# Kernel tuning notes

Measured on AMD Instinct MI355X. Metric: run time of the kernel, lower is better.

## Reference

```python
import jax, jax.numpy as jnp
import numpy as np

N_NODES = 50000
N_EDGES = 1600000
D = 64
F = 8
K = 16384


def setup_inputs() -> dict:
    key = jax.random.key(0)
    k1, k2, k3, k4, k5 = jax.random.split(key, 5)
    raw_data = jax.random.randint(k1, (N_NODES,), 0, F, dtype=jnp.int64) if jax.config.jax_enable_x64 else jax.random.randint(k1, (N_NODES,), 0, F, dtype=jnp.int32)
    edge_src = jax.random.randint(k2, (N_EDGES,), 0, N_NODES, dtype=jnp.int32)
    edge_dst = jax.random.randint(k3, (N_EDGES,), 0, N_NODES, dtype=jnp.int32)
    edge_vals = jax.random.normal(k4, (N_EDGES, D), dtype=jnp.float32)
    core_idxs = jax.random.randint(k5, (K,), 0, N_NODES, dtype=jnp.int32)
    return {
        "raw_data": raw_data,
        "edge_src": edge_src,
        "edge_dst": edge_dst,
        "edge_vals": edge_vals,
        "core_idxs": core_idxs,
        "feature_type_count": F,
    }


def reference(raw_data, edge_src, edge_dst, edge_vals, core_idxs, feature_type_count):
    # For each feature type f and origin node i:
    #   out[i, f, :] = max over edges (i -> j) of (edge_vals * [raw_data[j] == f])
    # Origins with no edges at all are zero (torch zero-init of max_res).
    n_nodes = raw_data.shape[0]
    dst_type = raw_data[edge_dst]  # [E] feature type of each edge's neighbor
    outs = []
    for f in range(feature_type_count):  # small fixed loop over feature types
        mask = (dst_type == f).astype(edge_vals.dtype)          # [E]
        masked = edge_vals * mask[:, None]                       # [E, D]
        seg = jax.ops.segment_max(masked, edge_src, num_segments=n_nodes)  # [N, D]
        seg = jnp.where(jnp.isneginf(seg), jnp.zeros((), seg.dtype), seg)  # empty origins -> 0
        outs.append(seg[core_idxs])                              # [K, D]
    return jnp.stack(outs, axis=1)  # [K, F, D]
```

## Files before the change

kernel.cpp:

```cpp
#include <hip/hip_runtime.h>

#define NNODES 50000
#define FT 8
#define DD 64
#define KK 16384
#define CAPF 16
#define OVFCAP 32768
#define NBW 1568


__global__ void init_kernel(int* __restrict__ cnt, int* __restrict__ bits,
                            int* __restrict__ head, int* __restrict__ gtot) {
    int i = blockIdx.x * 256 + threadIdx.x;
    if (i < NNODES * FT) cnt[i] = 0;
    if (i < NBW) bits[i] = 0;
    if (i < NNODES) head[i] = -1;
    if (i < 4) gtot[i] = 0;
}

__global__ void mark_kernel(const int* __restrict__ core, int* __restrict__ bits,
                            int* __restrict__ head, int* __restrict__ nxt,
                            int* __restrict__ slot_node, int* __restrict__ gtot) {
    int k = blockIdx.x * 256 + threadIdx.x;
    if (k >= KK) return;
    int node = core[k];
    nxt[k] = atomicExch(&head[node], k);
    unsigned bit = 1u << (node & 31);
    unsigned old = atomicOr((unsigned*)&bits[node >> 5], bit);
    if (!(old & bit)) {
        int s = atomicAdd(&gtot[1], 1);
        slot_node[s] = node;
    }
}

__global__ void scatter_kernel(const int4* __restrict__ esrc4, const int4* __restrict__ edst4,
                               const int* __restrict__ rawd, const int* __restrict__ bits,
                               int* __restrict__ cnt, int* __restrict__ sorted,
                               int* __restrict__ gtot, int* __restrict__ ovf_key,
                               int* __restrict__ ovf_e, int nE) {
    int t = blockIdx.x * 256 + threadIdx.x;
    int e = t * 4;
    if (e >= nE) return;
    if (e + 3 < nE) {
        int4 s = esrc4[t];
        int4 d = edst4[t];
        int sv[4] = {s.x, s.y, s.z, s.w};
        int dv[4] = {d.x, d.y, d.z, d.w};
#pragma unroll
        for (int j = 0; j < 4; ++j) {
            int sn = sv[j];
            if (!((((unsigned)bits[sn >> 5]) >> (sn & 31)) & 1u)) continue;
            int cell = sn * FT + rawd[dv[j]];
            int p = atomicAdd(&cnt[cell], 1);
            if (p < CAPF) {
                sorted[(size_t)cell * CAPF + p] = e + j;
            } else {
                int q = atomicAdd(&gtot[0], 1);
                if (q < OVFCAP) { ovf_key[q] = cell; ovf_e[q] = e + j; }
            }
        }
    } else {
        const int* esrc = (const int*)esrc4;
        const int* edst = (const int*)edst4;
        for (; e < nE; ++e) {
            int sn = esrc[e];
            if (!((((unsigned)bits[sn >> 5]) >> (sn & 31)) & 1u)) continue;
            int cell = sn * FT + rawd[edst[e]];
            int p = atomicAdd(&cnt[cell], 1);
            if (p < CAPF) {
                sorted[(size_t)cell * CAPF + p] = e;
            } else {
                int q = atomicAdd(&gtot[0], 1);
                if (q < OVFCAP) { ovf_key[q] = cell; ovf_e[q] = e; }
            }
        }
    }
}

#define RL(x) __builtin_amdgcn_readfirstlane(x)

__global__ void compute_kernel(const int* __restrict__ slot_node, const int* __restrict__ cnt,
                               const int* __restrict__ sorted, const int* __restrict__ head,
                               const int* __restrict__ nxt, const float* __restrict__ evals,
                               const int* __restrict__ gtot, const int* __restrict__ ovf_key,
                               const int* __restrict__ ovf_e, float* __restrict__ out) {
    int wave = (blockIdx.x * blockDim.x + threadIdx.x) >> 6;
    int lane = threadIdx.x & 63;
    if (wave >= gtot[1]) return;
    int node = RL(slot_node[wave]);

    const int4* c4 = (const int4*)(cnt + node * FT);
    int4 cA = c4[0], cB = c4[1];
    int cf[FT] = { RL(cA.x), RL(cA.y), RL(cA.z), RL(cA.w),
                   RL(cB.x), RL(cB.y), RL(cB.z), RL(cB.w) };
    int deg = 0;
    bool anyovf = false;
#pragma unroll
    for (int f = 0; f < FT; ++f) { deg += cf[f]; anyovf |= (cf[f] > CAPF); }

    const int4* bkt4 = (const int4*)(sorted + (size_t)node * FT * CAPF);
    int4 id0[FT], id1[FT];
#pragma unroll
    for (int f = 0; f < FT; ++f) { id0[f] = bkt4[f * 4]; id1[f] = bkt4[f * 4 + 1]; }

    float rmax[FT];
#pragma unroll
    for (int f = 0; f < FT; ++f) {
        int n = cf[f] < CAPF ? cf[f] : CAPF;
        float m0 = -INFINITY, m1 = -INFINITY, m2 = -INFINITY, m3 = -INFINITY;
        if (n > 0) m0 = evals[(size_t)RL(id0[f].x) * DD + lane];
        if (n > 1) m1 = evals[(size_t)RL(id0[f].y) * DD + lane];
        if (n > 2) m2 = evals[(size_t)RL(id0[f].z) * DD + lane];
        if (n > 3) m3 = evals[(size_t)RL(id0[f].w) * DD + lane];
        if (n > 4) m0 = fmaxf(m0, evals[(size_t)RL(id1[f].x) * DD + lane]);
        if (n > 5) m1 = fmaxf(m1, evals[(size_t)RL(id1[f].y) * DD + lane]);
        if (n > 6) m2 = fmaxf(m2, evals[(size_t)RL(id1[f].z) * DD + lane]);
        if (n > 7) m3 = fmaxf(m3, evals[(size_t)RL(id1[f].w) * DD + lane]);
        if (n > 8) {
            const int* bkt = sorted + ((size_t)node * FT + f) * CAPF;
            for (int i = 8; i < n; ++i)
                m0 = fmaxf(m0, evals[(size_t)RL(bkt[i]) * DD + lane]);
        }
        rmax[f] = fmaxf(fmaxf(m0, m1), fmaxf(m2, m3));
    }

    if (anyovf) {
        int no = gtot[0]; if (no > OVFCAP) no = OVFCAP;
        for (int q = 0; q < no; ++q) {
            int key = ovf_key[q];
            if ((key >> 3) != node) continue;
            int fo = key & 7;
            float v = evals[(size_t)ovf_e[q] * DD + lane];
#pragma unroll
            for (int t = 0; t < FT; ++t)
                if (t == fo) rmax[t] = fmaxf(rmax[t], v);
        }
    }

    float res[FT];
#pragma unroll
    for (int f = 0; f < FT; ++f) {
        int matched = cf[f];
        float val;
        if (matched == 0)        val = 0.0f;
        else if (matched < deg)  val = fmaxf(rmax[f], 0.0f);
        else                     val = rmax[f];
        res[f] = val;
    }

    for (int k = head[node]; k >= 0; k = nxt[k]) {
        float* op = out + (size_t)k * (FT * DD) + lane;
#pragma unroll
        for (int f = 0; f < FT; ++f) op[f * DD] = res[f];
    }
}

extern "C" void kernel_launch(void* const* d_in, const int* in_sizes, int n_in,
                              void* d_out, int out_size, void* d_ws, size_t ws_size,
                              hipStream_t stream) {
    const int*   rawd  = (const int*)d_in[0];
    const int*   esrc  = (const int*)d_in[1];
    const int*   edst  = (const int*)d_in[2];
    const float* evals = (const float*)d_in[3];
    const int*   core  = (const int*)d_in[4];
    int nE = in_sizes[1];

    int* wsi       = (int*)d_ws;
    int* cnt       = wsi;
    int* bits      = wsi + 400000;
    int* head      = wsi + 401568;
    int* nxt       = wsi + 451568;
    int* slot_node = wsi + 467952;
    int* gtot      = wsi + 484336;
    int* ovf_key   = wsi + 484340;
    int* ovf_e     = wsi + 517108;
    int* sorted    = wsi + 549888;

    init_kernel<<<(NNODES * FT + 255) / 256, 256, 0, stream>>>(cnt, bits, head, gtot);
    mark_kernel<<<(KK + 255) / 256, 256, 0, stream>>>(core, bits, head, nxt, slot_node, gtot);

    int nE4 = (nE + 3) / 4;
    scatter_kernel<<<(nE4 + 255) / 256, 256, 0, stream>>>(
        (const int4*)esrc, (const int4*)edst, rawd, bits, cnt, sorted,
        gtot, ovf_key, ovf_e, nE);

    long long cthreads = (long long)KK * 64;
    compute_kernel<<<(int)((cthreads + 255) / 256), 256, 0, stream>>>(
        slot_node, cnt, sorted, head, nxt, evals, gtot, ovf_key, ovf_e, (float*)d_out);
}
```

Measured before the change: 71.71 us.

## Replace init kernel with memset, drop slot list, widen scatter, use nontemporal accesses

Replaces the init kernel with a single hipMemsetAsync by storing linked-list heads offset by one, so zero means empty. Drops the compacted slot_node list: the compute kernel now launches one wave per node and exits early when the node's bitmap bit is clear. The scatter kernel handles 8 edges per thread instead of 4. Gathers of edge_vals and writes to the output use nontemporal load/store builtins. Together these cut a launch and some atomics, at the cost of launching about three times as many waves for compute, most of which exit immediately, and of worse ordering of node processing.

Measured after the change: 102.6 us. 1.43x slower.

```diff
diff --git a/kernel.cpp b/kernel.cpp
--- a/kernel.cpp
+++ b/kernel.cpp
@@ -9,47 +9,32 @@
 #define NBW 1568
 
 
-__global__ void init_kernel(int* __restrict__ cnt, int* __restrict__ bits,
-                            int* __restrict__ head, int* __restrict__ gtot) {
-    int i = blockIdx.x * 256 + threadIdx.x;
-    if (i < NNODES * FT) cnt[i] = 0;
-    if (i < NBW) bits[i] = 0;
-    if (i < NNODES) head[i] = -1;
-    if (i < 4) gtot[i] = 0;
-}
-
-__global__ void mark_kernel(const int* __restrict__ core, int* __restrict__ bits,
-                            int* __restrict__ head, int* __restrict__ nxt,
-                            int* __restrict__ slot_node, int* __restrict__ gtot) {
+__global__ void mark_kernel(const int* __restrict__ core, unsigned* __restrict__ bits,
+                            int* __restrict__ headp, int* __restrict__ nxtp) {
     int k = blockIdx.x * 256 + threadIdx.x;
     if (k >= KK) return;
     int node = core[k];
-    nxt[k] = atomicExch(&head[node], k);
-    unsigned bit = 1u << (node & 31);
-    unsigned old = atomicOr((unsigned*)&bits[node >> 5], bit);
-    if (!(old & bit)) {
-        int s = atomicAdd(&gtot[1], 1);
-        slot_node[s] = node;
-    }
+    nxtp[k] = atomicExch(&headp[node], k + 1);
+    atomicOr(&bits[node >> 5], 1u << (node & 31));
 }
 
 __global__ void scatter_kernel(const int4* __restrict__ esrc4, const int4* __restrict__ edst4,
-                               const int* __restrict__ rawd, const int* __restrict__ bits,
+                               const int* __restrict__ rawd, const unsigned* __restrict__ bits,
                                int* __restrict__ cnt, int* __restrict__ sorted,
                                int* __restrict__ gtot, int* __restrict__ ovf_key,
                                int* __restrict__ ovf_e, int nE) {
     int t = blockIdx.x * 256 + threadIdx.x;
-    int e = t * 4;
+    int e = t * 8;
     if (e >= nE) return;
-    if (e + 3 < nE) {
-        int4 s = esrc4[t];
-        int4 d = edst4[t];
-        int sv[4] = {s.x, s.y, s.z, s.w};
-        int dv[4] = {d.x, d.y, d.z, d.w};
+    if (e + 7 < nE) {
+        int4 sA = esrc4[t * 2], sB = esrc4[t * 2 + 1];
+        int4 dA = edst4[t * 2], dB = edst4[t * 2 + 1];
+        int sv[8] = {sA.x, sA.y, sA.z, sA.w, sB.x, sB.y, sB.z, sB.w};
+        int dv[8] = {dA.x, dA.y, dA.z, dA.w, dB.x, dB.y, dB.z, dB.w};
 #pragma unroll
-        for (int j = 0; j < 4; ++j) {
+        for (int j = 0; j < 8; ++j) {
             int sn = sv[j];
-            if (!((((unsigned)bits[sn >> 5]) >> (sn & 31)) & 1u)) continue;
+            if (!((bits[sn >> 5] >> (sn & 31)) & 1u)) continue;
             int cell = sn * FT + rawd[dv[j]];
             int p = atomicAdd(&cnt[cell], 1);
             if (p < CAPF) {
@@ -64,7 +49,7 @@
         const int* edst = (const int*)edst4;
         for (; e < nE; ++e) {
             int sn = esrc[e];
-            if (!((((unsigned)bits[sn >> 5]) >> (sn & 31)) & 1u)) continue;
+            if (!((bits[sn >> 5] >> (sn & 31)) & 1u)) continue;
             int cell = sn * FT + rawd[edst[e]];
             int p = atomicAdd(&cnt[cell], 1);
             if (p < CAPF) {
@@ -79,15 +64,15 @@
 
 #define RL(x) __builtin_amdgcn_readfirstlane(x)
 
-__global__ void compute_kernel(const int* __restrict__ slot_node, const int* __restrict__ cnt,
-                               const int* __restrict__ sorted, const int* __restrict__ head,
-                               const int* __restrict__ nxt, const float* __restrict__ evals,
+__global__ void compute_kernel(const unsigned* __restrict__ bits, const int* __restrict__ cnt,
+                               const int* __restrict__ sorted, const int* __restrict__ headp,
+                               const int* __restrict__ nxtp, const float* __restrict__ evals,
                                const int* __restrict__ gtot, const int* __restrict__ ovf_key,
                                const int* __restrict__ ovf_e, float* __restrict__ out) {
-    int wave = (blockIdx.x * blockDim.x + threadIdx.x) >> 6;
+    int node = (blockIdx.x * blockDim.x + threadIdx.x) >> 6;
     int lane = threadIdx.x & 63;
-    if (wave >= gtot[1]) return;
-    int node = RL(slot_node[wave]);
+    if (node >= NNODES) return;
+    if (!((bits[node >> 5] >> (node & 31)) & 1u)) return;
 
     const int4* c4 = (const int4*)(cnt + node * FT);
     int4 cA = c4[0], cB = c4[1];
@@ -108,18 +93,18 @@
     for (int f = 0; f < FT; ++f) {
         int n = cf[f] < CAPF ? cf[f] : CAPF;
         float m0 = -INFINITY, m1 = -INFINITY, m2 = -INFINITY, m3 = -INFINITY;
-        if (n > 0) m0 = evals[(size_t)RL(id0[f].x) * DD + lane];
-        if (n > 1) m1 = evals[(size_t)RL(id0[f].y) * DD + lane];
-        if (n > 2) m2 = evals[(size_t)RL(id0[f].z) * DD + lane];
-        if (n > 3) m3 = evals[(size_t)RL(id0[f].w) * DD + lane];
-        if (n > 4) m0 = fmaxf(m0, evals[(size_t)RL(id1[f].x) * DD + lane]);
-        if (n > 5) m1 = fmaxf(m1, evals[(size_t)RL(id1[f].y) * DD + lane]);
-        if (n > 6) m2 = fmaxf(m2, evals[(size_t)RL(id1[f].z) * DD + lane]);
-        if (n > 7) m3 = fmaxf(m3, evals[(size_t)RL(id1[f].w) * DD + lane]);
+        if (n > 0) m0 = __builtin_nontemporal_load(evals + (size_t)RL(id0[f].x) * DD + lane);
+        if (n > 1) m1 = __builtin_nontemporal_load(evals + (size_t)RL(id0[f].y) * DD + lane);
+        if (n > 2) m2 = __builtin_nontemporal_load(evals + (size_t)RL(id0[f].z) * DD + lane);
+        if (n > 3) m3 = __builtin_nontemporal_load(evals + (size_t)RL(id0[f].w) * DD + lane);
+        if (n > 4) m0 = fmaxf(m0, __builtin_nontemporal_load(evals + (size_t)RL(id1[f].x) * DD + lane));
+        if (n > 5) m1 = fmaxf(m1, __builtin_nontemporal_load(evals + (size_t)RL(id1[f].y) * DD + lane));
+        if (n > 6) m2 = fmaxf(m2, __builtin_nontemporal_load(evals + (size_t)RL(id1[f].z) * DD + lane));
+        if (n > 7) m3 = fmaxf(m3, __builtin_nontemporal_load(evals + (size_t)RL(id1[f].w) * DD + lane));
         if (n > 8) {
             const int* bkt = sorted + ((size_t)node * FT + f) * CAPF;
             for (int i = 8; i < n; ++i)
-                m0 = fmaxf(m0, evals[(size_t)RL(bkt[i]) * DD + lane]);
+                m0 = fmaxf(m0, __builtin_nontemporal_load(evals + (size_t)RL(bkt[i]) * DD + lane));
         }
         rmax[f] = fmaxf(fmaxf(m0, m1), fmaxf(m2, m3));
     }
@@ -148,10 +133,11 @@
         res[f] = val;
     }
 
-    for (int k = head[node]; k >= 0; k = nxt[k]) {
-        float* op = out + (size_t)k * (FT * DD) + lane;
+    for (int k1 = headp[node]; k1 > 0; k1 = nxtp[k1 - 1]) {
+        float* op = out + (size_t)(k1 - 1) * (FT * DD) + lane;
 #pragma unroll
-        for (int f = 0; f < FT; ++f) op[f * DD] = res[f];
+        for (int f = 0; f < FT; ++f)
+            __builtin_nontemporal_store(res[f], op + f * DD);
     }
 }
 
@@ -165,26 +151,26 @@
     const int*   core  = (const int*)d_in[4];
     int nE = in_sizes[1];
 
-    int* wsi       = (int*)d_ws;
-    int* cnt       = wsi;
-    int* bits      = wsi + 400000;
-    int* head      = wsi + 401568;
-    int* nxt       = wsi + 451568;
-    int* slot_node = wsi + 467952;
-    int* gtot      = wsi + 484336;
-    int* ovf_key   = wsi + 484340;
-    int* ovf_e     = wsi + 517108;
-    int* sorted    = wsi + 549888;
+    int* wsi      = (int*)d_ws;
+    int* cnt      = wsi;
+    unsigned* bits = (unsigned*)(wsi + 400000);
+    int* headp    = wsi + 401568;
+    int* gtot     = wsi + 451568;
+    int* nxtp     = wsi + 451572;
+    int* ovf_key  = wsi + 467956;
+    int* ovf_e    = wsi + 500724;
+    int* sorted   = wsi + 533504;
 
-    init_kernel<<<(NNODES * FT + 255) / 256, 256, 0, stream>>>(cnt, bits, head, gtot);
-    mark_kernel<<<(KK + 255) / 256, 256, 0, stream>>>(core, bits, head, nxt, slot_node, gtot);
+    hipMemsetAsync(d_ws, 0, (size_t)451572 * sizeof(int), stream);
 
-    int nE4 = (nE + 3) / 4;
-    scatter_kernel<<<(nE4 + 255) / 256, 256, 0, stream>>>(
+    mark_kernel<<<(KK + 255) / 256, 256, 0, stream>>>(core, bits, headp, nxtp);
+
+    int nE8 = (nE + 7) / 8;
+    scatter_kernel<<<(nE8 + 255) / 256, 256, 0, stream>>>(
         (const int4*)esrc, (const int4*)edst, rawd, bits, cnt, sorted,
         gtot, ovf_key, ovf_e, nE);
 
-    long long cthreads = (long long)KK * 64;
+    long long cthreads = (long long)NNODES * 64;
     compute_kernel<<<(int)((cthreads + 255) / 256), 256, 0, stream>>>(
-        slot_node, cnt, sorted, head, nxt, evals, gtot, ovf_key, ovf_e, (float*)d_out);
+        bits, cnt, sorted, headp, nxtp, evals, gtot, ovf_key, ovf_e, (float*)d_out);
 }
```
